# Optimization experiments

Hardware: AMD Instinct MI355X
Metric: run time of the kernel (lower is better)

## Reference

```python
import jax, jax.numpy as jnp
import numpy as np


def setup_inputs() -> dict:
    key = jax.random.key(0)
    k1, k2 = jax.random.split(key)
    B, N, D, F = 4, 50000, 64, 100000
    verts = jax.random.normal(k1, (B, N, D), dtype=jnp.float32)
    faces = jax.random.randint(k2, (B, F, 3), 0, N, dtype=jnp.int64)
    return {"verts": verts, "faces": faces}


def reference(verts, faces):
    # verts: [B, N, D], faces: [B, F, L] int indices into N
    B, N, D = verts.shape
    Ldeg = faces.shape[-1]
    # flatten batch into one block-diagonal graph, as the torch module does
    offset = (jnp.arange(B, dtype=faces.dtype) * N)[:, None, None]
    f = (faces + offset).reshape(-1, Ldeg)          # [B*F, L]
    row = f.reshape(-1)                              # f[:, 0..L-1]
    col = jnp.roll(f, -1, axis=1).reshape(-1)        # f[:, 1..L-1, 0]
    # L = L + L.T -> edges in both directions (duplicates accumulate)
    src = jnp.concatenate([row, col])
    dst = jnp.concatenate([col, row])
    Vf = verts.reshape(-1, D)                        # [B*N, D]
    # off-diagonal: -sum_j V_j over incident half-edges (with multiplicity)
    neigh = jax.ops.segment_sum(Vf[dst], src, num_segments=B * N)
    # Lii = degree (count of incident half-edges)
    deg = jax.ops.segment_sum(jnp.ones_like(src, dtype=verts.dtype), src,
                              num_segments=B * N)    # [B*N]
    # x = (Lii * V_i - sum_j V_j) / (Lii + eps)
    x = (deg[:, None] * Vf - neigh) / (deg[:, None] + 1e-12)
    return x.reshape(B, N, D)
```

## Files before the change

### kernel.cpp

```cpp
#include <hip/hip_runtime.h>
#include <hip/hip_fp16.h>

constexpr int Bc = 4;
constexpr int Nc = 50000;
constexpr int Dc = 64;
constexpr int Fc = 100000;
constexpr int BN = Bc * Nc;
constexpr int NFACES = Bc * Fc;
constexpr int NINC = NFACES * 3;
constexpr int CAP_E = 31;

constexpr int BINV_SH = 7;
constexpr int BINV    = 1 << BINV_SH;
constexpr int NBINS   = (BN + BINV - 1) / BINV;
constexpr int NBINS8  = ((NBINS + 7) / 8) * 8;
constexpr int BINCAP  = 1024;
constexpr int BINB    = 256;
constexpr int FPB     = (NFACES + BINB - 1) / BINB;
constexpr int CONVB   = (BN * Dc / 8) / 256;
constexpr unsigned int SENT = (unsigned)Nc | ((unsigned)Nc << 16);

constexpr size_t A_VH    = 0;
constexpr size_t A_ENT   = 25600512;
constexpr size_t A_BCUR  = A_ENT + (size_t)NBINS * BINCAP * 8;
constexpr size_t A3_NEED = A_BCUR + (size_t)NBINS * 32 * 4;

__global__ __launch_bounds__(256) void bin_conv(
        const float* __restrict__ verts,
        const int*   __restrict__ faces,
        __half* __restrict__ vh,
        int*   __restrict__ bincur,
        uint2* __restrict__ entries) {
    __shared__ unsigned int sfaces[FPB * 3];
    __shared__ int scnt[NBINS];
    __shared__ int sbase[NBINS];

    if ((int)blockIdx.x < BINB) {
        int blk = blockIdx.x, t = threadIdx.x;
        int f0g = blk * FPB;
        int nf  = NFACES - f0g; if (nf > FPB) nf = FPB;
        if (nf <= 0) return;

        for (int i = t; i < nf * 3; i += 256) sfaces[i] = (unsigned int)faces[f0g * 3 + i];
        for (int i = t; i < NBINS; i += 256) scnt[i] = 0;
        __syncthreads();

        for (int f = t; f < nf; f += 256) {
            int base = ((f0g + f) / Fc) * Nc;
            int g0 = (int)sfaces[3*f+0] + base;
            int g1 = (int)sfaces[3*f+1] + base;
            int g2 = (int)sfaces[3*f+2] + base;
            atomicAdd(&scnt[g0 >> BINV_SH], 1);
            atomicAdd(&scnt[g1 >> BINV_SH], 1);
            atomicAdd(&scnt[g2 >> BINV_SH], 1);
        }
        __syncthreads();

        for (int i = t; i < NBINS; i += 256) {
            int c = scnt[i];
            sbase[i] = (c > 0) ? atomicAdd(&bincur[i * 32], c) : 0;
            scnt[i] = 0;
        }
        __syncthreads();

        for (int f = t; f < nf; f += 256) {
            unsigned int u0 = sfaces[3*f+0];
            unsigned int u1 = sfaces[3*f+1];
            unsigned int u2 = sfaces[3*f+2];
            int base = ((f0g + f) / Fc) * Nc;
            int g0 = (int)u0 + base, g1 = (int)u1 + base, g2 = (int)u2 + base;
            int b0 = g0 >> BINV_SH, b1 = g1 >> BINV_SH, b2 = g2 >> BINV_SH;
            int p0 = sbase[b0] + atomicAdd(&scnt[b0], 1);
            if (p0 < BINCAP) entries[(size_t)b0 * BINCAP + p0] = make_uint2((unsigned)g0, u1 | (u2 << 16));
            int p1 = sbase[b1] + atomicAdd(&scnt[b1], 1);
            if (p1 < BINCAP) entries[(size_t)b1 * BINCAP + p1] = make_uint2((unsigned)g1, u0 | (u2 << 16));
            int p2 = sbase[b2] + atomicAdd(&scnt[b2], 1);
            if (p2 < BINCAP) entries[(size_t)b2 * BINCAP + p2] = make_uint2((unsigned)g2, u0 | (u1 << 16));
        }
    } else if ((int)blockIdx.x < BINB + CONVB) {
        long idx = ((long)(blockIdx.x - BINB) * 256 + threadIdx.x) * 8;
        int  v   = (int)(idx >> 6);
        int  b   = v / Nc;
        float4 a = *(const float4*)(verts + idx);
        float4 bb = *(const float4*)(verts + idx + 4);
        __half h[8];
        h[0] = __float2half(a.x);  h[1] = __float2half(a.y);
        h[2] = __float2half(a.z);  h[3] = __float2half(a.w);
        h[4] = __float2half(bb.x); h[5] = __float2half(bb.y);
        h[6] = __float2half(bb.z); h[7] = __float2half(bb.w);
        *(uint4*)(vh + idx + (long)b * 64) = *(const uint4*)h;
    } else {
        int t = threadIdx.x;
        if (t < 128) {
            int b = t >> 5, w = t & 31;
            ((unsigned int*)vh)[(long)(b * (Nc + 1) + Nc) * 32 + w] = 0u;
        }
    }
}

__global__ __launch_bounds__(256) void bucket_gather(
        const __half* __restrict__ vh,
        const uint2*  __restrict__ entries,
        const int*    __restrict__ bincur,
        float* __restrict__ out) {
    __shared__ unsigned int scnt[BINV];
    __shared__ unsigned int sent[BINV * 32];

    int d = blockIdx.x;
    int bin = (d >> 4) * 8 + (d & 7);
    int sub = (d >> 3) & 1;
    if (bin >= NBINS) return;
    int t = threadIdx.x;

    if (t < BINV) scnt[t] = 0;
    {
        uint4* s4 = (uint4*)sent;
        uint4 sv = make_uint4(SENT, SENT, SENT, SENT);
        for (int i = t; i < BINV * 32 / 4; i += 256) s4[i] = sv;
    }
    __syncthreads();

    int total = bincur[bin * 32];
    if (total > BINCAP) total = BINCAP;
    const uint2* e = entries + (size_t)bin * BINCAP;
    int v0 = bin << BINV_SH;
    for (int i = t; i < total; i += 256) {
        uint2 en = e[i];
        int vl = (int)en.x - v0;
        unsigned int r = atomicAdd(&scnt[vl], 1);
        if (r < (unsigned)CAP_E) sent[(vl << 5) + r] = en.y;
    }
    __syncthreads();

    int lane = t & 63, wv = t >> 6;
    int half = lane >> 5, j = lane & 31;
    const __half2* vh2 = (const __half2*)vh;
    int nrec = BN - v0; if (nrec > BINV) nrec = BINV;
    int vend = (sub + 1) << 6; if (vend > nrec) vend = nrec;

    for (int pair = (sub << 5) + wv; pair * 2 < vend; pair += 4) {
        int vl = pair * 2 + half;
        int v  = v0 + vl;
        int c  = (int)scnt[vl]; if (c > CAP_E) c = CAP_E;
        int cother = __shfl(c, lane ^ 32);
        int cmax = c > cother ? c : cother;
        int b = v / Nc;
        int base2 = b * (Nc + 1);

        float2 own = __half22float2(vh2[(v + b) * 32 + j]);

        const unsigned int* se = &sent[vl << 5];
        float accx = 0.f, accy = 0.f;
        for (int i = 0; i < cmax; i += 8) {
            unsigned int p0 = se[i];
            unsigned int p1 = se[i + 1];
            unsigned int p2 = se[i + 2];
            unsigned int p3 = se[i + 3];
            unsigned int p4 = se[i + 4];
            unsigned int p5 = se[i + 5];
            unsigned int p6 = se[i + 6];
            unsigned int p7 = se[i + 7];
            int r0  = (base2 + (int)(p0 & 0xFFFFu)) * 32 + j;
            int r1  = (base2 + (int)(p0 >> 16))     * 32 + j;
            int r2  = (base2 + (int)(p1 & 0xFFFFu)) * 32 + j;
            int r3  = (base2 + (int)(p1 >> 16))     * 32 + j;
            int r4  = (base2 + (int)(p2 & 0xFFFFu)) * 32 + j;
            int r5  = (base2 + (int)(p2 >> 16))     * 32 + j;
            int r6  = (base2 + (int)(p3 & 0xFFFFu)) * 32 + j;
            int r7  = (base2 + (int)(p3 >> 16))     * 32 + j;
            int r8  = (base2 + (int)(p4 & 0xFFFFu)) * 32 + j;
            int r9  = (base2 + (int)(p4 >> 16))     * 32 + j;
            int r10 = (base2 + (int)(p5 & 0xFFFFu)) * 32 + j;
            int r11 = (base2 + (int)(p5 >> 16))     * 32 + j;
            int r12 = (base2 + (int)(p6 & 0xFFFFu)) * 32 + j;
            int r13 = (base2 + (int)(p6 >> 16))     * 32 + j;
            int r14 = (base2 + (int)(p7 & 0xFFFFu)) * 32 + j;
            int r15 = (base2 + (int)(p7 >> 16))     * 32 + j;
            float2 f0  = __half22float2(vh2[r0]);
            float2 f1  = __half22float2(vh2[r1]);
            float2 f2  = __half22float2(vh2[r2]);
            float2 f3  = __half22float2(vh2[r3]);
            float2 f4  = __half22float2(vh2[r4]);
            float2 f5  = __half22float2(vh2[r5]);
            float2 f6  = __half22float2(vh2[r6]);
            float2 f7  = __half22float2(vh2[r7]);
            float2 f8  = __half22float2(vh2[r8]);
            float2 f9  = __half22float2(vh2[r9]);
            float2 f10 = __half22float2(vh2[r10]);
            float2 f11 = __half22float2(vh2[r11]);
            float2 f12 = __half22float2(vh2[r12]);
            float2 f13 = __half22float2(vh2[r13]);
            float2 f14 = __half22float2(vh2[r14]);
            float2 f15 = __half22float2(vh2[r15]);
            accx += ((f0.x + f1.x) + (f2.x + f3.x)) + ((f4.x + f5.x) + (f6.x + f7.x))
                  + ((f8.x + f9.x) + (f10.x + f11.x)) + ((f12.x + f13.x) + (f14.x + f15.x));
            accy += ((f0.y + f1.y) + (f2.y + f3.y)) + ((f4.y + f5.y) + (f6.y + f7.y))
                  + ((f8.y + f9.y) + (f10.y + f11.y)) + ((f12.y + f13.y) + (f14.y + f15.y));
        }

        float deg = 2.0f * (float)c;
        float den = deg + 1e-12f;
        float2 r;
        r.x = (deg * own.x - accx) / den;
        r.y = (deg * own.y - accy) / den;
        ((float2*)out)[(long)v * 32 + j] = r;
    }
}

constexpr size_t B_VH   = 0;
constexpr size_t B_REC  = 25600000;
constexpr size_t B_NEED = 51200000;
constexpr int FILLB = (NFACES + 255) / 256;

__global__ __launch_bounds__(256) void conv_fill(
        const float* __restrict__ verts,
        const int*   __restrict__ faces,
        __half* __restrict__ vh,
        unsigned int* __restrict__ rec) {
    if ((int)blockIdx.x < FILLB) {
        int f = blockIdx.x * 256 + threadIdx.x;
        if (f >= NFACES) return;
        int base = (f / Fc) * Nc;
        unsigned int u0 = (unsigned int)faces[3*f+0];
        unsigned int u1 = (unsigned int)faces[3*f+1];
        unsigned int u2 = (unsigned int)faces[3*f+2];
        unsigned int* r0 = rec + (long)((int)u0 + base) * 32;
        unsigned int* r1 = rec + (long)((int)u1 + base) * 32;
        unsigned int* r2 = rec + (long)((int)u2 + base) * 32;
        int s0 = atomicAdd((int*)r0, 1);
        if (s0 < CAP_E) r0[1 + s0] = u1 | (u2 << 16);
        int s1 = atomicAdd((int*)r1, 1);
        if (s1 < CAP_E) r1[1 + s1] = u0 | (u2 << 16);
        int s2 = atomicAdd((int*)r2, 1);
        if (s2 < CAP_E) r2[1 + s2] = u0 | (u1 << 16);
    } else {
        long idx = ((long)(blockIdx.x - FILLB) * 256 + threadIdx.x) * 8;
        float4 a = *(const float4*)(verts + idx);
        float4 b = *(const float4*)(verts + idx + 4);
        __half h[8];
        h[0] = __float2half(a.x); h[1] = __float2half(a.y);
        h[2] = __float2half(a.z); h[3] = __float2half(a.w);
        h[4] = __float2half(b.x); h[5] = __float2half(b.y);
        h[6] = __float2half(b.z); h[7] = __float2half(b.w);
        *(uint4*)(vh + idx) = *(const uint4*)h;
    }
}

__global__ __launch_bounds__(256) void gather2(
        const float*  __restrict__ verts,
        const __half* __restrict__ vh,
        const unsigned int* __restrict__ rec,
        float* __restrict__ out) {
    int gtid = blockIdx.x * 256 + threadIdx.x;
    int w    = gtid >> 6;
    int lane = threadIdx.x & 63;
    int half = lane >> 5;
    int j    = lane & 31;
    int v    = 2 * w + half;
    int h32  = half << 5;

    unsigned int rw = rec[(long)w * 64 + lane];
    int c = __shfl((int)rw, h32);
    if (c > CAP_E) c = CAP_E;
    int cother = __shfl(c, lane ^ 32);
    int cmax = c > cother ? c : cother;

    int base = (v / Nc) * Nc;
    const __half2* vh2 = (const __half2*)vh;
    float2 own = ((const float2*)verts)[(long)v * 32 + j];

    float accx = 0.f, accy = 0.f;
    for (int i = 0; i < cmax; i += 2) {
        unsigned int p0 = (unsigned int)__shfl((int)rw, h32 + 1 + i);
        unsigned int p1 = (unsigned int)__shfl((int)rw, h32 + 2 + i);
        float m0 = (i < c) ? 1.f : 0.f;
        float m1 = (i + 1 < c) ? 1.f : 0.f;
        unsigned int q0 = (i < c) ? p0 : 0u;
        unsigned int q1 = (i + 1 < c) ? p1 : 0u;
        long r0 = (long)(base + (int)(q0 & 0xFFFFu)) * 32 + j;
        long r1 = (long)(base + (int)(q0 >> 16))     * 32 + j;
        long r2 = (long)(base + (int)(q1 & 0xFFFFu)) * 32 + j;
        long r3 = (long)(base + (int)(q1 >> 16))     * 32 + j;
        float2 f0 = __half22float2(vh2[r0]);
        float2 f1 = __half22float2(vh2[r1]);
        float2 f2 = __half22float2(vh2[r2]);
        float2 f3 = __half22float2(vh2[r3]);
        accx += m0 * (f0.x + f1.x) + m1 * (f2.x + f3.x);
        accy += m0 * (f0.y + f1.y) + m1 * (f2.y + f3.y);
    }

    float deg = 2.0f * (float)c;
    float den = deg + 1e-12f;
    float2 r;
    r.x = (deg * own.x - accx) / den;
    r.y = (deg * own.y - accy) / den;
    ((float2*)out)[(long)v * 32 + j] = r;
}

constexpr int SCAN_ELEMS = 1024;
constexpr int NSCAN = (BN + SCAN_ELEMS - 1) / SCAN_ELEMS;
constexpr size_t WS_COUNTS  = 0;
constexpr size_t WS_OFFSETS = 800000;
constexpr size_t WS_CURSORS = 1600000;
constexpr size_t WS_BSUMS   = 2400000;
constexpr size_t WS_BBASE   = 2401024;
constexpr size_t WS_ENTRIES = 2402048;
constexpr size_t WS_NEEDED  = WS_ENTRIES + (size_t)NINC * 8;

__global__ __launch_bounds__(256) void count_kernel(
        const int* __restrict__ faces, int* __restrict__ counts) {
    int f = blockIdx.x * blockDim.x + threadIdx.x;
    if (f >= NFACES) return;
    int base = (f / Fc) * Nc;
    atomicAdd(&counts[faces[3*f+0] + base], 1);
    atomicAdd(&counts[faces[3*f+1] + base], 1);
    atomicAdd(&counts[faces[3*f+2] + base], 1);
}

__global__ __launch_bounds__(256) void scanA(
        const int* __restrict__ counts, int* __restrict__ bsums) {
    __shared__ int s[256];
    int t = threadIdx.x, b = blockIdx.x;
    int idx = b * SCAN_ELEMS + t * 4;
    int v = 0;
    if (idx + 4 <= BN) {
        int4 c = *(const int4*)(counts + idx);
        v = c.x + c.y + c.z + c.w;
    }
    s[t] = v; __syncthreads();
    for (int o = 128; o > 0; o >>= 1) {
        if (t < o) s[t] += s[t + o];
        __syncthreads();
    }
    if (t == 0) bsums[b] = s[0];
}

__global__ __launch_bounds__(256) void scanB(
        const int* __restrict__ bsums, int* __restrict__ bbase) {
    __shared__ int s[256];
    int t = threadIdx.x;
    int x = (t < NSCAN) ? bsums[t] : 0;
    s[t] = x; __syncthreads();
    for (int o = 1; o < 256; o <<= 1) {
        int v = (t >= o) ? s[t - o] : 0;
        __syncthreads();
        s[t] += v;
        __syncthreads();
    }
    bbase[t] = s[t] - x;
}

__global__ __launch_bounds__(256) void scanC(
        const int* __restrict__ counts, const int* __restrict__ bbase,
        int* __restrict__ offsets) {
    __shared__ int s[256];
    int t = threadIdx.x, b = blockIdx.x;
    int idx = b * SCAN_ELEMS + t * 4;
    int4 c = make_int4(0, 0, 0, 0);
    bool ok = (idx + 4 <= BN);
    if (ok) c = *(const int4*)(counts + idx);
    int tsum = c.x + c.y + c.z + c.w;
    s[t] = tsum; __syncthreads();
    for (int o = 1; o < 256; o <<= 1) {
        int v = (t >= o) ? s[t - o] : 0;
        __syncthreads();
        s[t] += v;
        __syncthreads();
    }
    int tbase = bbase[b] + s[t] - tsum;
    if (ok) {
        int4 o4;
        o4.x = tbase;
        o4.y = tbase + c.x;
        o4.z = tbase + c.x + c.y;
        o4.w = tbase + c.x + c.y + c.z;
        *(int4*)(offsets + idx) = o4;
    }
}

__global__ __launch_bounds__(256) void fill_kernel(
        const int* __restrict__ faces,
        const int* __restrict__ offsets,
        int* __restrict__ cursors,
        int2* __restrict__ entries) {
    int f = blockIdx.x * blockDim.x + threadIdx.x;
    if (f >= NFACES) return;
    int base = (f / Fc) * Nc;
    int v0 = faces[3*f+0] + base;
    int v1 = faces[3*f+1] + base;
    int v2 = faces[3*f+2] + base;
    int p0 = offsets[v0] + atomicAdd(&cursors[v0], 1);
    entries[p0] = make_int2(v1, v2);
    int p1 = offsets[v1] + atomicAdd(&cursors[v1], 1);
    entries[p1] = make_int2(v0, v2);
    int p2 = offsets[v2] + atomicAdd(&cursors[v2], 1);
    entries[p2] = make_int2(v0, v1);
}

__global__ __launch_bounds__(256) void gather_kernel(
        const float* __restrict__ verts,
        const int* __restrict__ counts,
        const int* __restrict__ offsets,
        const int2* __restrict__ entries,
        float* __restrict__ out) {
    int v    = (int)((blockIdx.x * blockDim.x + threadIdx.x) >> 6);
    int lane = threadIdx.x & 63;
    if (v >= BN) return;
    int c = counts[v];
    const int2* e = entries + offsets[v];
    float acc = 0.f;
    int i = 0;
    for (; i + 2 <= c; i += 2) {
        int2 a = e[i];
        int2 b = e[i + 1];
        acc += verts[(long)a.x * Dc + lane] + verts[(long)a.y * Dc + lane]
             + verts[(long)b.x * Dc + lane] + verts[(long)b.y * Dc + lane];
    }
    if (i < c) {
        int2 a = e[i];
        acc += verts[(long)a.x * Dc + lane] + verts[(long)a.y * Dc + lane];
    }
    float deg = 2.0f * (float)c;
    float own = verts[(long)v * Dc + lane];
    out[(long)v * Dc + lane] = (deg * own - acc) / (deg + 1e-12f);
}

extern "C" void kernel_launch(void* const* d_in, const int* in_sizes, int n_in,
                              void* d_out, int out_size, void* d_ws, size_t ws_size,
                              hipStream_t stream) {
    const float* verts = (const float*)d_in[0];
    const int*   faces = (const int*)d_in[1];
    float* out = (float*)d_out;
    char*  ws  = (char*)d_ws;

    if (ws_size >= A3_NEED) {
        __half*       vh      = (__half*)(ws + A_VH);
        uint2*        entries = (uint2*)(ws + A_ENT);
        int*          bincur  = (int*)(ws + A_BCUR);

        hipMemsetAsync(bincur, 0, (size_t)NBINS * 32 * sizeof(int), stream);
        bin_conv<<<BINB + CONVB + 1, 256, 0, stream>>>(verts, faces, vh, bincur, entries);
        bucket_gather<<<NBINS8 * 2, 256, 0, stream>>>(vh, entries, bincur, out);
    } else if (ws_size >= B_NEED) {
        __half*       vh  = (__half*)(ws + B_VH);
        unsigned int* rec = (unsigned int*)(ws + B_REC);
        hipMemsetAsync(rec, 0, (size_t)BN * 32 * sizeof(unsigned int), stream);
        conv_fill<<<FILLB + CONVB, 256, 0, stream>>>(verts, faces, vh, rec);
        gather2<<<BN * 32 / 256, 256, 0, stream>>>(verts, vh, rec, out);
    } else if (ws_size >= WS_NEEDED) {
        int*  counts  = (int*)(ws + WS_COUNTS);
        int*  offsets = (int*)(ws + WS_OFFSETS);
        int*  cursors = (int*)(ws + WS_CURSORS);
        int*  bsums   = (int*)(ws + WS_BSUMS);
        int*  bbase   = (int*)(ws + WS_BBASE);
        int2* entries = (int2*)(ws + WS_ENTRIES);

        hipMemsetAsync(counts,  0, (size_t)BN * sizeof(int), stream);
        hipMemsetAsync(cursors, 0, (size_t)BN * sizeof(int), stream);
        int fb = (NFACES + 255) / 256;
        count_kernel<<<fb, 256, 0, stream>>>(faces, counts);
        scanA<<<NSCAN, 256, 0, stream>>>(counts, bsums);
        scanB<<<1, 256, 0, stream>>>(bsums, bbase);
        scanC<<<NSCAN, 256, 0, stream>>>(counts, bbase, offsets);
        fill_kernel<<<fb, 256, 0, stream>>>(faces, offsets, cursors, entries);
        int gb = (BN * 64 + 255) / 256;
        gather_kernel<<<gb, 256, 0, stream>>>(verts, counts, offsets, entries, out);
    }
}
```

Baseline: 157.8 us.

## Fuse memset, bin/convert and gather into one cooperative persistent kernel

Replaces the memset plus two kernel launches with a single cooperative kernel that zeroes counters, runs the binning/fp16 conversion phase, and then the bucket-gather phase, separated by grid-wide syncs. Blocks pull work items from atomic job queues instead of one block per job. This aims to remove launch gaps and the separate memset. In exchange it adds grid.sync costs, global atomic queue contention, and a limited persistent grid that may lower occupancy. The old path is kept as a fallback if the cooperative launch fails.

```diff
diff --git a/kernel.cpp b/kernel.cpp
--- a/kernel.cpp
+++ b/kernel.cpp
@@ -1,5 +1,8 @@
 #include <hip/hip_runtime.h>
 #include <hip/hip_fp16.h>
+#include <hip/hip_cooperative_groups.h>
+
+namespace cg = cooperative_groups;
 
 constexpr int Bc = 4;
 constexpr int Nc = 50000;
@@ -18,12 +21,210 @@
 constexpr int BINB    = 256;
 constexpr int FPB     = (NFACES + BINB - 1) / BINB;
 constexpr int CONVB   = (BN * Dc / 8) / 256;
+constexpr int NJOBS1  = BINB + CONVB + 1;
+constexpr int NJOBS2  = NBINS8 * 2;
 constexpr unsigned int SENT = (unsigned)Nc | ((unsigned)Nc << 16);
 
 constexpr size_t A_VH    = 0;
 constexpr size_t A_ENT   = 25600512;
 constexpr size_t A_BCUR  = A_ENT + (size_t)NBINS * BINCAP * 8;
-constexpr size_t A3_NEED = A_BCUR + (size_t)NBINS * 32 * 4;
+constexpr size_t A_Q     = A_BCUR + (size_t)NBINS * 32 * 4;
+constexpr size_t A3_NEED = A_Q + 256;
+
+__global__ __launch_bounds__(256) void fused_all(
+        const float* __restrict__ verts,
+        const int*   __restrict__ faces,
+        __half* __restrict__ vh,
+        int*   __restrict__ bincur,
+        uint2* __restrict__ entries,
+        int*   __restrict__ q,
+        float* __restrict__ out) {
+    __shared__ union {
+        struct { int scnt[NBINS]; int sbase[NBINS]; } bs;
+        struct { unsigned int scnt[BINV]; unsigned int sent[BINV * 32]; } gs;
+    } sh;
+    __shared__ int sjob;
+
+    cg::grid_group grid = cg::this_grid();
+    int t    = threadIdx.x;
+    int gtid = blockIdx.x * 256 + t;
+    int nth  = gridDim.x * 256;
+
+    for (int i = gtid; i < NBINS * 32; i += nth) bincur[i] = 0;
+    if (gtid < 64) q[gtid] = 0;
+    grid.sync();
+
+    for (;;) {
+        __syncthreads();
+        if (t == 0) sjob = atomicAdd(&q[0], 1);
+        __syncthreads();
+        int job = sjob;
+        if (job >= NJOBS1) break;
+
+        if (job < BINB) {
+            int f0g = job * FPB;
+            int nf  = NFACES - f0g; if (nf > FPB) nf = FPB;
+            for (int i = t; i < NBINS; i += 256) sh.bs.scnt[i] = 0;
+            __syncthreads();
+            for (int f = t; f < nf; f += 256) {
+                int fg   = f0g + f;
+                int base = (fg / Fc) * Nc;
+                int g0 = faces[3*fg+0] + base;
+                int g1 = faces[3*fg+1] + base;
+                int g2 = faces[3*fg+2] + base;
+                atomicAdd(&sh.bs.scnt[g0 >> BINV_SH], 1);
+                atomicAdd(&sh.bs.scnt[g1 >> BINV_SH], 1);
+                atomicAdd(&sh.bs.scnt[g2 >> BINV_SH], 1);
+            }
+            __syncthreads();
+            for (int i = t; i < NBINS; i += 256) {
+                int c = sh.bs.scnt[i];
+                sh.bs.sbase[i] = (c > 0) ? atomicAdd(&bincur[i * 32], c) : 0;
+                sh.bs.scnt[i] = 0;
+            }
+            __syncthreads();
+            for (int f = t; f < nf; f += 256) {
+                int fg   = f0g + f;
+                int base = (fg / Fc) * Nc;
+                unsigned int u0 = (unsigned int)faces[3*fg+0];
+                unsigned int u1 = (unsigned int)faces[3*fg+1];
+                unsigned int u2 = (unsigned int)faces[3*fg+2];
+                int g0 = (int)u0 + base, g1 = (int)u1 + base, g2 = (int)u2 + base;
+                int b0 = g0 >> BINV_SH, b1 = g1 >> BINV_SH, b2 = g2 >> BINV_SH;
+                int p0 = sh.bs.sbase[b0] + atomicAdd(&sh.bs.scnt[b0], 1);
+                if (p0 < BINCAP) entries[(size_t)b0 * BINCAP + p0] = make_uint2((unsigned)g0, u1 | (u2 << 16));
+                int p1 = sh.bs.sbase[b1] + atomicAdd(&sh.bs.scnt[b1], 1);
+                if (p1 < BINCAP) entries[(size_t)b1 * BINCAP + p1] = make_uint2((unsigned)g1, u0 | (u2 << 16));
+                int p2 = sh.bs.sbase[b2] + atomicAdd(&sh.bs.scnt[b2], 1);
+                if (p2 < BINCAP) entries[(size_t)b2 * BINCAP + p2] = make_uint2((unsigned)g2, u0 | (u1 << 16));
+            }
+        } else if (job < BINB + CONVB) {
+            long idx = ((long)(job - BINB) * 256 + t) * 8;
+            int  v   = (int)(idx >> 6);
+            int  b   = v / Nc;
+            float4 a  = *(const float4*)(verts + idx);
+            float4 bb = *(const float4*)(verts + idx + 4);
+            __half h[8];
+            h[0] = __float2half(a.x);  h[1] = __float2half(a.y);
+            h[2] = __float2half(a.z);  h[3] = __float2half(a.w);
+            h[4] = __float2half(bb.x); h[5] = __float2half(bb.y);
+            h[6] = __float2half(bb.z); h[7] = __float2half(bb.w);
+            *(uint4*)(vh + idx + (long)b * 64) = *(const uint4*)h;
+        } else {
+            if (t < 128) {
+                int b = t >> 5, w = t & 31;
+                ((unsigned int*)vh)[(long)(b * (Nc + 1) + Nc) * 32 + w] = 0u;
+            }
+        }
+    }
+    grid.sync();
+
+    const __half2* vh2 = (const __half2*)vh;
+    int lane = t & 63, wv = t >> 6;
+    int half = lane >> 5, j = lane & 31;
+
+    for (;;) {
+        __syncthreads();
+        if (t == 0) sjob = atomicAdd(&q[32], 1);
+        __syncthreads();
+        int d = sjob;
+        if (d >= NJOBS2) break;
+        int bin = (d >> 4) * 8 + (d & 7);
+        int sub = (d >> 3) & 1;
+        if (bin >= NBINS) continue;
+
+        if (t < BINV) sh.gs.scnt[t] = 0;
+        {
+            uint4* s4 = (uint4*)sh.gs.sent;
+            uint4 sv = make_uint4(SENT, SENT, SENT, SENT);
+            for (int i = t; i < BINV * 32 / 4; i += 256) s4[i] = sv;
+        }
+        __syncthreads();
+
+        int total = bincur[bin * 32];
+        if (total > BINCAP) total = BINCAP;
+        const uint2* e = entries + (size_t)bin * BINCAP;
+        int v0 = bin << BINV_SH;
+        for (int i = t; i < total; i += 256) {
+            uint2 en = e[i];
+            int vl = (int)en.x - v0;
+            unsigned int r = atomicAdd(&sh.gs.scnt[vl], 1);
+            if (r < (unsigned)CAP_E) sh.gs.sent[(vl << 5) + r] = en.y;
+        }
+        __syncthreads();
+
+        int nrec = BN - v0; if (nrec > BINV) nrec = BINV;
+        int vend = (sub + 1) << 6; if (vend > nrec) vend = nrec;
+
+        for (int pair = (sub << 5) + wv; pair * 2 < vend; pair += 4) {
+            int vl = pair * 2 + half;
+            int v  = v0 + vl;
+            int c  = (int)sh.gs.scnt[vl]; if (c > CAP_E) c = CAP_E;
+            int cother = __shfl(c, lane ^ 32);
+            int cmax = c > cother ? c : cother;
+            int b = v / Nc;
+            int base2 = b * (Nc + 1);
+
+            float2 own = __half22float2(vh2[(v + b) * 32 + j]);
+
+            const unsigned int* se = &sh.gs.sent[vl << 5];
+            float accx = 0.f, accy = 0.f;
+            for (int i = 0; i < cmax; i += 8) {
+                unsigned int p0 = se[i];
+                unsigned int p1 = se[i + 1];
+                unsigned int p2 = se[i + 2];
+                unsigned int p3 = se[i + 3];
+                unsigned int p4 = se[i + 4];
+                unsigned int p5 = se[i + 5];
+                unsigned int p6 = se[i + 6];
+                unsigned int p7 = se[i + 7];
+                int r0  = (base2 + (int)(p0 & 0xFFFFu)) * 32 + j;
+                int r1  = (base2 + (int)(p0 >> 16))     * 32 + j;
+                int r2  = (base2 + (int)(p1 & 0xFFFFu)) * 32 + j;
+                int r3  = (base2 + (int)(p1 >> 16))     * 32 + j;
+                int r4  = (base2 + (int)(p2 & 0xFFFFu)) * 32 + j;
+                int r5  = (base2 + (int)(p2 >> 16))     * 32 + j;
+                int r6  = (base2 + (int)(p3 & 0xFFFFu)) * 32 + j;
+                int r7  = (base2 + (int)(p3 >> 16))     * 32 + j;
+                int r8  = (base2 + (int)(p4 & 0xFFFFu)) * 32 + j;
+                int r9  = (base2 + (int)(p4 >> 16))     * 32 + j;
+                int r10 = (base2 + (int)(p5 & 0xFFFFu)) * 32 + j;
+                int r11 = (base2 + (int)(p5 >> 16))     * 32 + j;
+                int r12 = (base2 + (int)(p6 & 0xFFFFu)) * 32 + j;
+                int r13 = (base2 + (int)(p6 >> 16))     * 32 + j;
+                int r14 = (base2 + (int)(p7 & 0xFFFFu)) * 32 + j;
+                int r15 = (base2 + (int)(p7 >> 16))     * 32 + j;
+                float2 f0  = __half22float2(vh2[r0]);
+                float2 f1  = __half22float2(vh2[r1]);
+                float2 f2  = __half22float2(vh2[r2]);
+                float2 f3  = __half22float2(vh2[r3]);
+                float2 f4  = __half22float2(vh2[r4]);
+                float2 f5  = __half22float2(vh2[r5]);
+                float2 f6  = __half22float2(vh2[r6]);
+                float2 f7  = __half22float2(vh2[r7]);
+                float2 f8  = __half22float2(vh2[r8]);
+                float2 f9  = __half22float2(vh2[r9]);
+                float2 f10 = __half22float2(vh2[r10]);
+                float2 f11 = __half22float2(vh2[r11]);
+                float2 f12 = __half22float2(vh2[r12]);
+                float2 f13 = __half22float2(vh2[r13]);
+                float2 f14 = __half22float2(vh2[r14]);
+                float2 f15 = __half22float2(vh2[r15]);
+                accx += ((f0.x + f1.x) + (f2.x + f3.x)) + ((f4.x + f5.x) + (f6.x + f7.x))
+                      + ((f8.x + f9.x) + (f10.x + f11.x)) + ((f12.x + f13.x) + (f14.x + f15.x));
+                accy += ((f0.y + f1.y) + (f2.y + f3.y)) + ((f4.y + f5.y) + (f6.y + f7.y))
+                      + ((f8.y + f9.y) + (f10.y + f11.y)) + ((f12.y + f13.y) + (f14.y + f15.y));
+            }
+
+            float deg = 2.0f * (float)c;
+            float den = deg + 1e-12f;
+            float2 r;
+            r.x = (deg * own.x - accx) / den;
+            r.y = (deg * own.y - accy) / den;
+            ((float2*)out)[(long)v * 32 + j] = r;
+        }
+    }
+}
 
 __global__ __launch_bounds__(256) void bin_conv(
         const float* __restrict__ verts,
@@ -437,10 +638,28 @@
         __half*       vh      = (__half*)(ws + A_VH);
         uint2*        entries = (uint2*)(ws + A_ENT);
         int*          bincur  = (int*)(ws + A_BCUR);
-
-        hipMemsetAsync(bincur, 0, (size_t)NBINS * 32 * sizeof(int), stream);
-        bin_conv<<<BINB + CONVB + 1, 256, 0, stream>>>(verts, faces, vh, bincur, entries);
-        bucket_gather<<<NBINS8 * 2, 256, 0, stream>>>(vh, entries, bincur, out);
+        int*          q       = (int*)(ws + A_Q);
+
+        static int coopGrid = 0;
+        if (coopGrid == 0) {
+            int perCU = 0;
+            hipError_t oe = hipOccupancyMaxActiveBlocksPerMultiprocessor(
+                    &perCU, reinterpret_cast<const void*>(&fused_all), 256, 0);
+            if (oe != hipSuccess || perCU <= 0) perCU = 4;
+            coopGrid = perCU * 256;
+            if (coopGrid > 4096) coopGrid = 4096;
+        }
+
+        void* args[] = {(void*)&verts, (void*)&faces, (void*)&vh,
+                        (void*)&bincur, (void*)&entries, (void*)&q, (void*)&out};
+        hipError_t e = hipLaunchCooperativeKernel(
+                reinterpret_cast<const void*>(&fused_all),
+                dim3(coopGrid), dim3(256), args, 0, stream);
+        if (e != hipSuccess) {
+            hipMemsetAsync(bincur, 0, (size_t)NBINS * 32 * sizeof(int), stream);
+            bin_conv<<<BINB + CONVB + 1, 256, 0, stream>>>(verts, faces, vh, bincur, entries);
+            bucket_gather<<<NBINS8 * 2, 256, 0, stream>>>(vh, entries, bincur, out);
+        }
     } else if (ws_size >= B_NEED) {
         __half*       vh  = (__half*)(ws + B_VH);
         unsigned int* rec = (unsigned int*)(ws + B_REC);
```

Measured after the change: 384.3 us. +143.5%, slower.
